# Performance work log

Measured on AMD Instinct MI355X. Metric: run time of the kernel, lower is better.

Reference implementation:

```python
import jax, jax.numpy as jnp
import numpy as np

N = 50000
D = 128
E = 600000

def setup_inputs() -> dict:
    key = jax.random.key(0)
    k1, k2, k3, k4, k5 = jax.random.split(key, 5)
    z1 = jax.random.normal(k1, (N, D), dtype=jnp.float32)
    z2 = jax.random.normal(k2, (N, D), dtype=jnp.float32)
    adj_row = jax.random.randint(k3, (E,), 0, N, dtype=jnp.int32)
    adj_col = jax.random.randint(k4, (E,), 0, N, dtype=jnp.int32)
    adj_val = jax.random.uniform(k5, (E,), dtype=jnp.float32)
    a = jnp.full((N, D), 0.5, dtype=jnp.float32)
    b = jnp.full((N, D), 0.5, dtype=jnp.float32)
    alpha = jnp.float32(0.5)
    return {"z1": z1, "z2": z2, "adj_row": adj_row, "adj_col": adj_col,
            "adj_val": adj_val, "a": a, "b": b, "alpha": alpha}

def reference(z1, z2, adj_row, adj_col, adj_val, a, b, alpha):
    # elementwise gated combine: z_i = a*z1 + b*z2   [N, D]
    z_i = a * z1 + b * z2
    # sparse matmul: z_l[r] = sum_e adj_val[e] * z_i[adj_col[e]] for adj_row[e]==r
    msgs = adj_val[:, None] * z_i[adj_col]          # [E, D]
    z_l = jax.ops.segment_sum(msgs, adj_row, num_segments=N)  # [N, D]
    # residual blend
    return alpha * z_l + (1.0 - alpha) * z_i
```

## Files before the change

kernel.cpp:

```cpp
#include <hip/hip_runtime.h>

#define DDIM 128
#define CAPMAX 32

__global__ void __launch_bounds__(256) build_kernel(
    const float4* __restrict__ z1, const float4* __restrict__ z2,
    const float4* __restrict__ a,  const float4* __restrict__ b,
    float4* __restrict__ zi, int n4,
    const int* __restrict__ rows, const int* __restrict__ cols,
    const float* __restrict__ vals,
    int2* __restrict__ slots, int* __restrict__ cnt,
    int* __restrict__ ohead, int* __restrict__ onext,
    int cap, int E) {
  const int i = blockIdx.x * blockDim.x + threadIdx.x;
  const int stride = gridDim.x * blockDim.x;
  for (int j = i; j < n4; j += stride) {
    float4 A = a[j], B = b[j], X = z1[j], Y = z2[j];
    float4 z;
    z.x = A.x * X.x + B.x * Y.x;
    z.y = A.y * X.y + B.y * Y.y;
    z.z = A.z * X.z + B.z * Y.z;
    z.w = A.w * X.w + B.w * Y.w;
    zi[j] = z;
  }
  for (int e = i; e < E; e += stride) {
    const int r = rows[e];
    const int j = atomicAdd(&cnt[r], 1);
    if (j < cap) {
      int2 s;
      s.x = cols[e];
      s.y = __float_as_int(vals[e]);
      slots[(size_t)r * cap + j] = s;
    } else {
      onext[e] = atomicExch(&ohead[r], e);
    }
  }
}

__global__ void __launch_bounds__(256) reduce_kernel(
    const int2* __restrict__ slots, const int* __restrict__ cnt,
    const int* __restrict__ ohead, const int* __restrict__ onext,
    const int* __restrict__ cols, const float* __restrict__ vals,
    const float* __restrict__ alpha_p,
    const float2* __restrict__ zi2, float2* __restrict__ out2,
    int cap, int N) {
  const int r = (int)((blockIdx.x * blockDim.x + threadIdx.x) >> 6);
  const int lane = threadIdx.x & 63;
  if (r >= N) return;
  const float alpha = alpha_p[0];

  const int deg = cnt[r];
  const int m = deg < cap ? deg : cap;
  const int2* sp = slots + (size_t)r * cap;
  const int4* sp4 = (const int4*)sp;

  float2 acc0 = make_float2(0.f, 0.f), acc1 = acc0, acc2 = acc0, acc3 = acc0;
  int j = 0;
  for (; j + 4 <= m; j += 4) {
    const int4 p0 = sp4[j >> 1];
    const int4 p1 = sp4[(j >> 1) + 1];
    const float2 g0 = zi2[(size_t)p0.x * (DDIM / 2) + lane];
    const float2 g1 = zi2[(size_t)p0.z * (DDIM / 2) + lane];
    const float2 g2 = zi2[(size_t)p1.x * (DDIM / 2) + lane];
    const float2 g3 = zi2[(size_t)p1.z * (DDIM / 2) + lane];
    const float v0 = __int_as_float(p0.y), v1 = __int_as_float(p0.w);
    const float v2 = __int_as_float(p1.y), v3 = __int_as_float(p1.w);
    acc0.x += v0 * g0.x; acc0.y += v0 * g0.y;
    acc1.x += v1 * g1.x; acc1.y += v1 * g1.y;
    acc2.x += v2 * g2.x; acc2.y += v2 * g2.y;
    acc3.x += v3 * g3.x; acc3.y += v3 * g3.y;
  }
  for (; j < m; ++j) {
    const int2 s = sp[j];
    const float v = __int_as_float(s.y);
    const float2 g = zi2[(size_t)s.x * (DDIM / 2) + lane];
    acc0.x += v * g.x; acc0.y += v * g.y;
  }
  if (deg > cap) {
    int e = ohead[r];
    while (e >= 0) {
      const int en = onext[e];
      const int c = cols[e];
      const float v = vals[e];
      const float2 g = zi2[(size_t)c * (DDIM / 2) + lane];
      acc0.x += v * g.x; acc0.y += v * g.y;
      e = en;
    }
  }

  float2 acc;
  acc.x = (acc0.x + acc1.x) + (acc2.x + acc3.x);
  acc.y = (acc0.y + acc1.y) + (acc2.y + acc3.y);
  const float2 zr = zi2[(size_t)r * (DDIM / 2) + lane];
  const float om = 1.0f - alpha;
  float2 o;
  o.x = alpha * acc.x + om * zr.x;
  o.y = alpha * acc.y + om * zr.y;
  out2[(size_t)r * (DDIM / 2) + lane] = o;
}

extern "C" void kernel_launch(void* const* d_in, const int* in_sizes, int n_in,
                              void* d_out, int out_size, void* d_ws, size_t ws_size,
                              hipStream_t stream) {
  const float* z1    = (const float*)d_in[0];
  const float* z2    = (const float*)d_in[1];
  const int*   rows  = (const int*)  d_in[2];
  const int*   cols  = (const int*)  d_in[3];
  const float* vals  = (const float*)d_in[4];
  const float* a     = (const float*)d_in[5];
  const float* b     = (const float*)d_in[6];
  const float* alpha = (const float*)d_in[7];
  float* out = (float*)d_out;

  const int ND = in_sizes[0];
  const int E  = in_sizes[2];
  const int N  = ND / DDIM;
  const int n4 = ND / 4;

  float* zi  = (float*)d_ws;
  int* cnt   = (int*)(zi + ND);
  int* ohead = cnt + N;
  int* onext = ohead + N;
  int2* slots = (int2*)(onext + E);

  const size_t fixed_bytes = ((size_t)ND + 2 * N + E) * 4;
  size_t avail = ws_size > fixed_bytes ? ws_size - fixed_bytes : 0;
  int cap = (int)(avail / ((size_t)N * sizeof(int2)));
  if (cap > CAPMAX) cap = CAPMAX;
  cap &= ~1;
  if (cap < 2) cap = 0;

  hipMemsetAsync(cnt, 0x00, (size_t)N * sizeof(int), stream);
  hipMemsetAsync(ohead, 0xFF, (size_t)N * sizeof(int), stream);

  build_kernel<<<2048, 256, 0, stream>>>(
      (const float4*)z1, (const float4*)z2, (const float4*)a,
      (const float4*)b, (float4*)zi, n4,
      rows, cols, vals, slots, cnt, ohead, onext, cap, E);

  const int blocks2 = (int)(((long long)N * 64 + 255) / 256);
  reduce_kernel<<<blocks2, 256, 0, stream>>>(
      slots, cnt, ohead, onext, cols, vals, alpha,
      (const float2*)zi, (float2*)out, cap, N);
}
```

Baseline: 212.6 us.

## Gather fp16 copy of combined features and split build kernel roles

The build kernel now also writes a half-precision copy of z_i. The reduce kernel gathers neighbour rows from that copy, halving gather bandwidth, and keeps fp32 only for the residual term. Build blocks are split by parity so half do the elementwise combine and half do edge bucketing. The gather loop is unrolled to 8 edges, and the overflow list now encodes index+1 so a single memset zeroes both cnt and ohead. Accumulating from fp16 values adds rounding error that may exceed the tolerance.

```diff
diff --git a/kernel.cpp b/kernel.cpp
--- a/kernel.cpp
+++ b/kernel.cpp
@@ -1,4 +1,5 @@
 #include <hip/hip_runtime.h>
+#include <hip/hip_fp16.h>
 
 #define DDIM 128
 #define CAPMAX 32
@@ -6,33 +7,42 @@
 __global__ void __launch_bounds__(256) build_kernel(
     const float4* __restrict__ z1, const float4* __restrict__ z2,
     const float4* __restrict__ a,  const float4* __restrict__ b,
-    float4* __restrict__ zi, int n4,
+    float4* __restrict__ zi32, uint2* __restrict__ zi16, int n4,
     const int* __restrict__ rows, const int* __restrict__ cols,
     const float* __restrict__ vals,
     int2* __restrict__ slots, int* __restrict__ cnt,
     int* __restrict__ ohead, int* __restrict__ onext,
     int cap, int E) {
-  const int i = blockIdx.x * blockDim.x + threadIdx.x;
-  const int stride = gridDim.x * blockDim.x;
-  for (int j = i; j < n4; j += stride) {
-    float4 A = a[j], B = b[j], X = z1[j], Y = z2[j];
-    float4 z;
-    z.x = A.x * X.x + B.x * Y.x;
-    z.y = A.y * X.y + B.y * Y.y;
-    z.z = A.z * X.z + B.z * Y.z;
-    z.w = A.w * X.w + B.w * Y.w;
-    zi[j] = z;
-  }
-  for (int e = i; e < E; e += stride) {
-    const int r = rows[e];
-    const int j = atomicAdd(&cnt[r], 1);
-    if (j < cap) {
-      int2 s;
-      s.x = cols[e];
-      s.y = __float_as_int(vals[e]);
-      slots[(size_t)r * cap + j] = s;
-    } else {
-      onext[e] = atomicExch(&ohead[r], e);
+  const int t = (blockIdx.x >> 1) * blockDim.x + threadIdx.x;
+  const int stride = (gridDim.x >> 1) * blockDim.x;
+  if (blockIdx.x & 1) {
+    for (int e = t; e < E; e += stride) {
+      const int r = rows[e];
+      const int j = atomicAdd(&cnt[r], 1);
+      if (j < cap) {
+        int2 s;
+        s.x = cols[e];
+        s.y = __float_as_int(vals[e]);
+        slots[(size_t)r * cap + j] = s;
+      } else {
+        onext[e] = atomicExch(&ohead[r], e + 1);
+      }
+    }
+  } else {
+    for (int j = t; j < n4; j += stride) {
+      float4 A = a[j], B = b[j], X = z1[j], Y = z2[j];
+      float4 z;
+      z.x = A.x * X.x + B.x * Y.x;
+      z.y = A.y * X.y + B.y * Y.y;
+      z.z = A.z * X.z + B.z * Y.z;
+      z.w = A.w * X.w + B.w * Y.w;
+      zi32[j] = z;
+      __half2 h0 = __floats2half2_rn(z.x, z.y);
+      __half2 h1 = __floats2half2_rn(z.z, z.w);
+      uint2 pk;
+      pk.x = *reinterpret_cast<unsigned*>(&h0);
+      pk.y = *reinterpret_cast<unsigned*>(&h1);
+      zi16[j] = pk;
     }
   }
 }
@@ -42,8 +52,8 @@
     const int* __restrict__ ohead, const int* __restrict__ onext,
     const int* __restrict__ cols, const float* __restrict__ vals,
     const float* __restrict__ alpha_p,
-    const float2* __restrict__ zi2, float2* __restrict__ out2,
-    int cap, int N) {
+    const __half2* __restrict__ zi16, const float2* __restrict__ zi32,
+    float2* __restrict__ out2, int cap, int N) {
   const int r = (int)((blockIdx.x * blockDim.x + threadIdx.x) >> 6);
   const int lane = threadIdx.x & 63;
   if (r >= N) return;
@@ -54,44 +64,61 @@
   const int2* sp = slots + (size_t)r * cap;
   const int4* sp4 = (const int4*)sp;
 
-  float2 acc0 = make_float2(0.f, 0.f), acc1 = acc0, acc2 = acc0, acc3 = acc0;
+  float2 a0 = make_float2(0.f, 0.f), a1 = a0, a2 = a0, a3 = a0;
+  float2 a4 = a0, a5 = a0, a6 = a0, a7 = a0;
   int j = 0;
-  for (; j + 4 <= m; j += 4) {
-    const int4 p0 = sp4[j >> 1];
+  for (; j + 8 <= m; j += 8) {
+    const int4 p0 = sp4[(j >> 1) + 0];
     const int4 p1 = sp4[(j >> 1) + 1];
-    const float2 g0 = zi2[(size_t)p0.x * (DDIM / 2) + lane];
-    const float2 g1 = zi2[(size_t)p0.z * (DDIM / 2) + lane];
-    const float2 g2 = zi2[(size_t)p1.x * (DDIM / 2) + lane];
-    const float2 g3 = zi2[(size_t)p1.z * (DDIM / 2) + lane];
+    const int4 p2 = sp4[(j >> 1) + 2];
+    const int4 p3 = sp4[(j >> 1) + 3];
+    const __half2 g0 = zi16[(size_t)p0.x * (DDIM / 2) + lane];
+    const __half2 g1 = zi16[(size_t)p0.z * (DDIM / 2) + lane];
+    const __half2 g2 = zi16[(size_t)p1.x * (DDIM / 2) + lane];
+    const __half2 g3 = zi16[(size_t)p1.z * (DDIM / 2) + lane];
+    const __half2 g4 = zi16[(size_t)p2.x * (DDIM / 2) + lane];
+    const __half2 g5 = zi16[(size_t)p2.z * (DDIM / 2) + lane];
+    const __half2 g6 = zi16[(size_t)p3.x * (DDIM / 2) + lane];
+    const __half2 g7 = zi16[(size_t)p3.z * (DDIM / 2) + lane];
+    const float2 f0 = __half22float2(g0), f1 = __half22float2(g1);
+    const float2 f2 = __half22float2(g2), f3 = __half22float2(g3);
+    const float2 f4 = __half22float2(g4), f5 = __half22float2(g5);
+    const float2 f6 = __half22float2(g6), f7 = __half22float2(g7);
     const float v0 = __int_as_float(p0.y), v1 = __int_as_float(p0.w);
     const float v2 = __int_as_float(p1.y), v3 = __int_as_float(p1.w);
-    acc0.x += v0 * g0.x; acc0.y += v0 * g0.y;
-    acc1.x += v1 * g1.x; acc1.y += v1 * g1.y;
-    acc2.x += v2 * g2.x; acc2.y += v2 * g2.y;
-    acc3.x += v3 * g3.x; acc3.y += v3 * g3.y;
+    const float v4 = __int_as_float(p2.y), v5 = __int_as_float(p2.w);
+    const float v6 = __int_as_float(p3.y), v7 = __int_as_float(p3.w);
+    a0.x += v0 * f0.x; a0.y += v0 * f0.y;
+    a1.x += v1 * f1.x; a1.y += v1 * f1.y;
+    a2.x += v2 * f2.x; a2.y += v2 * f2.y;
+    a3.x += v3 * f3.x; a3.y += v3 * f3.y;
+    a4.x += v4 * f4.x; a4.y += v4 * f4.y;
+    a5.x += v5 * f5.x; a5.y += v5 * f5.y;
+    a6.x += v6 * f6.x; a6.y += v6 * f6.y;
+    a7.x += v7 * f7.x; a7.y += v7 * f7.y;
   }
   for (; j < m; ++j) {
     const int2 s = sp[j];
     const float v = __int_as_float(s.y);
-    const float2 g = zi2[(size_t)s.x * (DDIM / 2) + lane];
-    acc0.x += v * g.x; acc0.y += v * g.y;
+    const float2 f = __half22float2(zi16[(size_t)s.x * (DDIM / 2) + lane]);
+    a0.x += v * f.x; a0.y += v * f.y;
   }
   if (deg > cap) {
-    int e = ohead[r];
-    while (e >= 0) {
-      const int en = onext[e];
+    int e1 = ohead[r];
+    while (e1 > 0) {
+      const int e = e1 - 1;
+      e1 = onext[e];
       const int c = cols[e];
       const float v = vals[e];
-      const float2 g = zi2[(size_t)c * (DDIM / 2) + lane];
-      acc0.x += v * g.x; acc0.y += v * g.y;
-      e = en;
+      const float2 f = __half22float2(zi16[(size_t)c * (DDIM / 2) + lane]);
+      a0.x += v * f.x; a0.y += v * f.y;
     }
   }
 
   float2 acc;
-  acc.x = (acc0.x + acc1.x) + (acc2.x + acc3.x);
-  acc.y = (acc0.y + acc1.y) + (acc2.y + acc3.y);
-  const float2 zr = zi2[(size_t)r * (DDIM / 2) + lane];
+  acc.x = ((a0.x + a1.x) + (a2.x + a3.x)) + ((a4.x + a5.x) + (a6.x + a7.x));
+  acc.y = ((a0.y + a1.y) + (a2.y + a3.y)) + ((a4.y + a5.y) + (a6.y + a7.y));
+  const float2 zr = zi32[(size_t)r * (DDIM / 2) + lane];
   const float om = 1.0f - alpha;
   float2 o;
   o.x = alpha * acc.x + om * zr.x;
@@ -117,29 +144,30 @@
   const int N  = ND / DDIM;
   const int n4 = ND / 4;
 
-  float* zi  = (float*)d_ws;
-  int* cnt   = (int*)(zi + ND);
+  float* zi32 = (float*)d_ws;
+  __half2* zi16 = (__half2*)(zi32 + ND);
+  int* cnt   = (int*)((char*)zi16 + (size_t)ND * 2);
   int* ohead = cnt + N;
   int* onext = ohead + N;
   int2* slots = (int2*)(onext + E);
 
-  const size_t fixed_bytes = ((size_t)ND + 2 * N + E) * 4;
+  const size_t fixed_bytes = (size_t)ND * 4 + (size_t)ND * 2 +
+                             ((size_t)2 * N + E) * 4;
   size_t avail = ws_size > fixed_bytes ? ws_size - fixed_bytes : 0;
   int cap = (int)(avail / ((size_t)N * sizeof(int2)));
   if (cap > CAPMAX) cap = CAPMAX;
   cap &= ~1;
   if (cap < 2) cap = 0;
 
-  hipMemsetAsync(cnt, 0x00, (size_t)N * sizeof(int), stream);
-  hipMemsetAsync(ohead, 0xFF, (size_t)N * sizeof(int), stream);
+  hipMemsetAsync(cnt, 0x00, (size_t)2 * N * sizeof(int), stream);
 
   build_kernel<<<2048, 256, 0, stream>>>(
       (const float4*)z1, (const float4*)z2, (const float4*)a,
-      (const float4*)b, (float4*)zi, n4,
+      (const float4*)b, (float4*)zi32, (uint2*)zi16, n4,
       rows, cols, vals, slots, cnt, ohead, onext, cap, E);
 
   const int blocks2 = (int)(((long long)N * 64 + 255) / 256);
   reduce_kernel<<<blocks2, 256, 0, stream>>>(
       slots, cnt, ohead, onext, cols, vals, alpha,
-      (const float2*)zi, (float2*)out, cap, N);
+      zi16, (const float2*)zi32, (float2*)out, cap, N);
 }
```

After: 199.6 us. -6.1%, faster.
